# Optimization experiments

Measured on AMD Instinct MI355X. Metric: run time of the kernel, lower is better.

The kernel has to match this reference:

```python
import jax, jax.numpy as jnp
import numpy as np

DIM = 768
HEADS = 12
HEAD_DIM = DIM // HEADS


def setup_inputs() -> dict:
    key = jax.random.key(0)
    ks = jax.random.split(key, 6)
    B, N = 8, 1024
    x = jax.random.normal(ks[0], (B, N, DIM), dtype=jnp.float32)
    # Linear weights stored as (in, out) so y = x @ W + b (equiv to torch x @ W.T)
    w_qkv = jax.random.normal(ks[1], (DIM, 3 * DIM), dtype=jnp.float32) * 0.02
    b_qkv = jnp.zeros((3 * DIM,), dtype=jnp.float32)
    w_proj = jax.random.normal(ks[2], (DIM, DIM), dtype=jnp.float32) * 0.02
    b_proj = jnp.zeros((DIM,), dtype=jnp.float32)
    temperature = jnp.ones((HEADS, 1, 1), dtype=jnp.float32)
    return {"x": x, "w_qkv": w_qkv, "b_qkv": b_qkv, "w_proj": w_proj,
            "b_proj": b_proj, "temperature": temperature}


def reference(x, w_qkv, b_qkv, w_proj, b_proj, temperature):
    B, N, C = x.shape
    qkv = x @ w_qkv + b_qkv                                  # (B,N,3C)
    qkv = qkv.reshape(B, N, 3, HEADS, HEAD_DIM)
    q = qkv[:, :, 0].transpose(0, 2, 1, 3)                    # (B,H,N,D)
    k = qkv[:, :, 1].transpose(0, 2, 1, 3)
    v = qkv[:, :, 2].transpose(0, 2, 1, 3)
    # LSA: learnable per-head temperature instead of 1/sqrt(d)
    scores = jnp.einsum('bhnd,bhmd->bhnm', q, k) * temperature  # temp broadcasts over (h,1,1)
    # diagonal mask: no self-attention
    diag = jnp.eye(N, dtype=bool)
    scores = jnp.where(diag, -jnp.inf, scores)
    attn = jax.nn.softmax(scores, axis=-1)                    # dropout p=0 (eval)
    out = jnp.einsum('bhnm,bhmd->bhnd', attn, v)              # (B,H,N,D)
    out = out.transpose(0, 2, 1, 3).reshape(B, N, C)
    return out @ w_proj + b_proj
```

## Files before the change

kernel.cpp:

```cpp
#include <hip/hip_runtime.h>
#include <hip/hip_bf16.h>


typedef __attribute__((ext_vector_type(8))) short bf16x8;
typedef __attribute__((ext_vector_type(4))) float f32x4;

__device__ __forceinline__ unsigned short f2bf(float f) {
    union { float f; unsigned u; } v; v.f = f;
    unsigned r = v.u + 0x7fff + ((v.u >> 16) & 1);
    return (unsigned short)(r >> 16);
}

__device__ __forceinline__ void gl_lds16(const unsigned short* g, unsigned short* l) {
    __builtin_amdgcn_global_load_lds(
        (const __attribute__((address_space(1))) void*)g,
        (__attribute__((address_space(3))) void*)l, 16, 0, 0);
}

__device__ __forceinline__ bf16x8 rd_sw(const unsigned short* lds, int row, int chunk) {
    return *(const bf16x8*)&lds[row * 64 + (((chunk ^ (row & 7))) << 3)];
}

__device__ __forceinline__ void stage64(const unsigned short* g, int gstride,
                                        unsigned short* lds, int t) {
    int row0 = t >> 3, c = t & 7;
    #pragma unroll
    for (int r = 0; r < 2; r++) {
        int row = r * 32 + row0;
        gl_lds16(g + (size_t)row * gstride + ((c ^ (row & 7)) << 3),
                 lds + r * 2048 + ((t >> 6) << 9));
    }
}

__global__ void pack_x(const float* __restrict__ src, unsigned short* __restrict__ dst, int n4) {
    int i = blockIdx.x * blockDim.x + threadIdx.x;
    if (i < n4) {
        float4 v = ((const float4*)src)[i];
        ushort4 o;
        o.x = f2bf(v.x); o.y = f2bf(v.y); o.z = f2bf(v.z); o.w = f2bf(v.w);
        ((ushort4*)dst)[i] = o;
    }
}

__global__ void transpose_pack(const float* __restrict__ src, unsigned short* __restrict__ dst,
                               int R, int C) {
    __shared__ float tile[64][65];
    int t = threadIdx.x;
    int c0 = blockIdx.x * 64, r0 = blockIdx.y * 64;
    int tr = t >> 4, tc4 = (t & 15) * 4;
    #pragma unroll
    for (int p = 0; p < 4; p++) {
        int r = tr + p * 16;
        float4 v = *(const float4*)&src[(size_t)(r0 + r) * C + c0 + tc4];
        tile[r][tc4 + 0] = v.x; tile[r][tc4 + 1] = v.y;
        tile[r][tc4 + 2] = v.z; tile[r][tc4 + 3] = v.w;
    }
    __syncthreads();
    #pragma unroll
    for (int p = 0; p < 4; p++) {
        int rr = tr + p * 16;
        ushort4 o;
        o.x = f2bf(tile[tc4 + 0][rr]);
        o.y = f2bf(tile[tc4 + 1][rr]);
        o.z = f2bf(tile[tc4 + 2][rr]);
        o.w = f2bf(tile[tc4 + 3][rr]);
        *(ushort4*)&dst[(size_t)(c0 + rr) * R + r0 + tc4] = o;
    }
}

__global__ __launch_bounds__(256, 2)
void gemm_qkv(const unsigned short* __restrict__ xb, const unsigned short* __restrict__ wT,
              const float* __restrict__ bias,
              unsigned short* __restrict__ qb, unsigned short* __restrict__ kb,
              unsigned short* __restrict__ vb) {
    const int K = 768;
    __shared__ unsigned short As[8192];
    __shared__ unsigned short Bs[8192];
    int t = threadIdx.x;
    int m0 = blockIdx.x * 128;
    int n0 = blockIdx.y * 128;
    int w = t >> 6, lane = t & 63, l16 = lane & 15, quad = lane >> 4;
    int wm = w >> 1, wn = w & 1;
    const f32x4 zero4 = {0.f, 0.f, 0.f, 0.f};
    f32x4 acc[4][4];
    #pragma unroll
    for (int a = 0; a < 4; a++)
        #pragma unroll
        for (int b = 0; b < 4; b++) acc[a][b] = zero4;

    int row0 = t >> 3, ch = t & 7;
    const unsigned short* gA = xb + (size_t)m0 * K;
    const unsigned short* gB = wT + (size_t)n0 * K;

    for (int k0 = 0; k0 < K; k0 += 64) {
        __syncthreads();
        #pragma unroll
        for (int r = 0; r < 4; r++) {
            int row = r * 32 + row0;
            int gc = k0 + ((ch ^ (row & 7)) << 3);
            gl_lds16(gA + (size_t)row * K + gc, As + r * 2048 + ((t >> 6) << 9));
            gl_lds16(gB + (size_t)row * K + gc, Bs + r * 2048 + ((t >> 6) << 9));
        }
        __syncthreads();
        #pragma unroll
        for (int ks = 0; ks < 2; ks++) {
            bf16x8 af[4], bf[4];
            #pragma unroll
            for (int mi = 0; mi < 4; mi++)
                af[mi] = rd_sw(As, wm * 64 + mi * 16 + l16, ks * 4 + quad);
            #pragma unroll
            for (int ni = 0; ni < 4; ni++)
                bf[ni] = rd_sw(Bs, wn * 64 + ni * 16 + l16, ks * 4 + quad);
            #pragma unroll
            for (int mi = 0; mi < 4; mi++)
                #pragma unroll
                for (int ni = 0; ni < 4; ni++)
                    acc[mi][ni] = __builtin_amdgcn_mfma_f32_16x16x32_bf16(af[mi], bf[ni], acc[mi][ni], 0, 0, 0);
        }
    }

    int nb = n0 + wn * 64;
    int seg = nb / 768;
    int nc = nb % 768;
    int h = nc >> 6;
    int bb = m0 >> 10;
    int bh = bb * 12 + h;
    float bv[4];
    #pragma unroll
    for (int ni = 0; ni < 4; ni++) bv[ni] = bias[nb + ni * 16 + l16];

    if (seg < 2) {
        unsigned short* dst = (seg == 0) ? qb : kb;
        #pragma unroll
        for (int mi = 0; mi < 4; mi++) {
            int nrow_base = (m0 & 1023) + wm * 64 + mi * 16 + quad * 4;
            #pragma unroll
            for (int i = 0; i < 4; i++) {
                unsigned short* drow = dst + ((size_t)bh * 1024 + nrow_base + i) * 64;
                #pragma unroll
                for (int ni = 0; ni < 4; ni++)
                    drow[ni * 16 + l16] = f2bf(acc[mi][ni][i] + bv[ni]);
            }
        }
    } else {
        #pragma unroll
        for (int mi = 0; mi < 4; mi++) {
            int nrow0 = (m0 & 1023) + wm * 64 + mi * 16 + quad * 4;
            #pragma unroll
            for (int ni = 0; ni < 4; ni++) {
                int d = ni * 16 + l16;
                ushort4 pk;
                pk.x = f2bf(acc[mi][ni][0] + bv[ni]);
                pk.y = f2bf(acc[mi][ni][1] + bv[ni]);
                pk.z = f2bf(acc[mi][ni][2] + bv[ni]);
                pk.w = f2bf(acc[mi][ni][3] + bv[ni]);
                *(ushort4*)&vb[((size_t)bh * 64 + d) * 1024 + nrow0] = pk;
            }
        }
    }
}

__global__ __launch_bounds__(256, 4)
void attn_kernel(const unsigned short* __restrict__ qb, const unsigned short* __restrict__ kb,
                 const unsigned short* __restrict__ vb, const float* __restrict__ temp,
                 unsigned short* __restrict__ attn) {
    __shared__ unsigned short Kt[2][4096];
    __shared__ unsigned short Vt[2][4096];
    __shared__ unsigned short Ps[4][1024];
    int t = threadIdx.x, w = t >> 6, lane = t & 63, l16 = lane & 15, quad = lane >> 4;
    int bh = blockIdx.x, qblk = blockIdx.y;
    int bb = bh / 12, h = bh % 12;
    float tscale = temp[h] * 1.44269504088896f;
    int qbase = qblk * 64 + w * 16;

    const unsigned short* kbase = kb + (size_t)bh * 65536;
    const unsigned short* vbase = vb + (size_t)bh * 65536;

    stage64(kbase, 64, Kt[0], t);
    stage64(vbase, 1024, Vt[0], t);

    const unsigned short* qrow = qb + ((size_t)bh * 1024 + qbase + l16) * 64;
    bf16x8 bq0 = *(const bf16x8*)&qrow[quad * 8];
    bf16x8 bq1 = *(const bf16x8*)&qrow[32 + quad * 8];

    bf16x8 aone;
    #pragma unroll
    for (int j = 0; j < 8; j++) aone[j] = (short)0x3F80;

    const f32x4 zero4 = {0.f, 0.f, 0.f, 0.f};
    f32x4 Oacc[4];
    f32x4 Osum = zero4;
    #pragma unroll
    for (int ti = 0; ti < 4; ti++) Oacc[ti] = zero4;

    unsigned short* pw = Ps[w];

    int bw_[4];
    #pragma unroll
    for (int ni = 0; ni < 4; ni++) {
        int qp = ni * 2 + (quad >> 1);
        bw_[ni] = qp * 128 + ((l16 + 2 * qp) & 15) * 8 + (quad & 1) * 4;
    }
    int qp0 = quad, qp1 = 4 + quad;
    int br0 = qp0 * 128 + ((l16 + 2 * qp0) & 15) * 8;
    int br1 = qp1 * 128 + ((l16 + 2 * qp1) & 15) * 8;

    bool eq[4];
    #pragma unroll
    for (int i = 0; i < 4; i++) eq[i] = (l16 == quad * 4 + i);

    for (int kt = 0; kt < 16; kt++) {
        int cur = kt & 1;
        __syncthreads();
        if (kt < 15) {
            stage64(kbase + (size_t)(kt + 1) * 4096, 64, Kt[cur ^ 1], t);
            stage64(vbase + (size_t)(kt + 1) * 64, 1024, Vt[cur ^ 1], t);
        }
        const unsigned short* Kc = Kt[cur];
        const unsigned short* Vc = Vt[cur];

        #pragma unroll
        for (int ni = 0; ni < 4; ni++) {
            bf16x8 ak0 = rd_sw(Kc, ni * 16 + l16, quad);
            bf16x8 ak1 = rd_sw(Kc, ni * 16 + l16, 4 + quad);
            f32x4 z = zero4;
            z = __builtin_amdgcn_mfma_f32_16x16x32_bf16(ak0, bq0, z, 0, 0, 0);
            z = __builtin_amdgcn_mfma_f32_16x16x32_bf16(ak1, bq1, z, 0, 0, 0);
            bool dw = (kt == qblk) && (ni == w);
            float p0 = exp2f(z[0] * tscale);
            float p1 = exp2f(z[1] * tscale);
            float p2 = exp2f(z[2] * tscale);
            float p3 = exp2f(z[3] * tscale);
            if (dw) {
                if (eq[0]) p0 = 0.f;
                if (eq[1]) p1 = 0.f;
                if (eq[2]) p2 = 0.f;
                if (eq[3]) p3 = 0.f;
            }
            union { ushort4 u; __hip_bfloat162 h[2]; } pk;
            pk.h[0] = __float22bfloat162_rn(make_float2(p0, p1));
            pk.h[1] = __float22bfloat162_rn(make_float2(p2, p3));
            *(ushort4*)&pw[bw_[ni]] = pk.u;
        }

        bf16x8 pt0 = *(const bf16x8*)&pw[br0];
        bf16x8 pt1 = *(const bf16x8*)&pw[br1];

        Osum = __builtin_amdgcn_mfma_f32_16x16x32_bf16(aone, pt0, Osum, 0, 0, 0);
        Osum = __builtin_amdgcn_mfma_f32_16x16x32_bf16(aone, pt1, Osum, 0, 0, 0);

        #pragma unroll
        for (int ti = 0; ti < 4; ti++) {
            bf16x8 av0 = rd_sw(Vc, ti * 16 + l16, quad);
            bf16x8 av1 = rd_sw(Vc, ti * 16 + l16, 4 + quad);
            Oacc[ti] = __builtin_amdgcn_mfma_f32_16x16x32_bf16(av0, pt0, Oacc[ti], 0, 0, 0);
            Oacc[ti] = __builtin_amdgcn_mfma_f32_16x16x32_bf16(av1, pt1, Oacc[ti], 0, 0, 0);
        }
    }

    float inv = 1.0f / Osum[0];
    int orow = bb * 1024 + qbase + l16;
    #pragma unroll
    for (int ti = 0; ti < 4; ti++) {
        union { ushort4 u; __hip_bfloat162 h[2]; } pk;
        pk.h[0] = __float22bfloat162_rn(make_float2(Oacc[ti][0] * inv, Oacc[ti][1] * inv));
        pk.h[1] = __float22bfloat162_rn(make_float2(Oacc[ti][2] * inv, Oacc[ti][3] * inv));
        int col = h * 64 + ti * 16 + quad * 4;
        *(ushort4*)&attn[(size_t)orow * 768 + col] = pk.u;
    }
}

__global__ __launch_bounds__(256, 2)
void gemm_proj(const unsigned short* __restrict__ ab, const unsigned short* __restrict__ wT,
               const float* __restrict__ bias, float* __restrict__ out) {
    const int K = 768;
    __shared__ unsigned short As[8192];
    __shared__ unsigned short Bs[8192];
    int t = threadIdx.x;
    int m0 = blockIdx.x * 128;
    int n0 = blockIdx.y * 128;
    int w = t >> 6, lane = t & 63, l16 = lane & 15, quad = lane >> 4;
    int wm = w >> 1, wn = w & 1;
    const f32x4 zero4 = {0.f, 0.f, 0.f, 0.f};
    f32x4 acc[4][4];
    #pragma unroll
    for (int a = 0; a < 4; a++)
        #pragma unroll
        for (int b = 0; b < 4; b++) acc[a][b] = zero4;

    int row0 = t >> 3, ch = t & 7;
    const unsigned short* gA = ab + (size_t)m0 * K;
    const unsigned short* gB = wT + (size_t)n0 * K;

    for (int k0 = 0; k0 < K; k0 += 64) {
        __syncthreads();
        #pragma unroll
        for (int r = 0; r < 4; r++) {
            int row = r * 32 + row0;
            int gc = k0 + ((ch ^ (row & 7)) << 3);
            gl_lds16(gA + (size_t)row * K + gc, As + r * 2048 + ((t >> 6) << 9));
            gl_lds16(gB + (size_t)row * K + gc, Bs + r * 2048 + ((t >> 6) << 9));
        }
        __syncthreads();
        #pragma unroll
        for (int ks = 0; ks < 2; ks++) {
            bf16x8 af[4], bf[4];
            #pragma unroll
            for (int mi = 0; mi < 4; mi++)
                af[mi] = rd_sw(As, wm * 64 + mi * 16 + l16, ks * 4 + quad);
            #pragma unroll
            for (int ni = 0; ni < 4; ni++)
                bf[ni] = rd_sw(Bs, wn * 64 + ni * 16 + l16, ks * 4 + quad);
            #pragma unroll
            for (int mi = 0; mi < 4; mi++)
                #pragma unroll
                for (int ni = 0; ni < 4; ni++)
                    acc[mi][ni] = __builtin_amdgcn_mfma_f32_16x16x32_bf16(af[mi], bf[ni], acc[mi][ni], 0, 0, 0);
        }
    }

    #pragma unroll
    for (int mi = 0; mi < 4; mi++)
        #pragma unroll
        for (int i = 0; i < 4; i++) {
            int row = m0 + wm * 64 + mi * 16 + quad * 4 + i;
            float* orow = out + (size_t)row * 768;
            #pragma unroll
            for (int ni = 0; ni < 4; ni++) {
                int col = n0 + wn * 64 + ni * 16 + l16;
                orow[col] = acc[mi][ni][i] + bias[col];
            }
        }
}

extern "C" void kernel_launch(void* const* d_in, const int* in_sizes, int n_in,
                              void* d_out, int out_size, void* d_ws, size_t ws_size,
                              hipStream_t stream) {
    const float* x      = (const float*)d_in[0];
    const float* w_qkv  = (const float*)d_in[1];
    const float* b_qkv  = (const float*)d_in[2];
    const float* w_proj = (const float*)d_in[3];
    const float* b_proj = (const float*)d_in[4];
    const float* temp   = (const float*)d_in[5];
    float* out = (float*)d_out;

    char* ws = (char*)d_ws;
    unsigned short* xb     = (unsigned short*)(ws);
    unsigned short* wqkvT  = (unsigned short*)(ws + 12582912);
    unsigned short* wprojT = (unsigned short*)(ws + 16121856);
    unsigned short* qb     = (unsigned short*)(ws + 17301504);
    unsigned short* kb     = (unsigned short*)(ws + 29884416);
    unsigned short* vb     = (unsigned short*)(ws + 42467328);
    unsigned short* attn   = (unsigned short*)(ws + 55050240);

    pack_x<<<6144, 256, 0, stream>>>(x, xb, 1572864);
    transpose_pack<<<dim3(36, 12), 256, 0, stream>>>(w_qkv, wqkvT, 768, 2304);
    transpose_pack<<<dim3(12, 12), 256, 0, stream>>>(w_proj, wprojT, 768, 768);
    gemm_qkv<<<dim3(64, 18), 256, 0, stream>>>(xb, wqkvT, b_qkv, qb, kb, vb);
    attn_kernel<<<dim3(96, 16), 256, 0, stream>>>(qb, kb, vb, temp, attn);
    gemm_proj<<<dim3(64, 6), 256, 0, stream>>>(attn, wprojT, b_proj, out);
}
```

Baseline: 208.2 us.

## Keep softmax probabilities in registers, double query rows per warp, fuse prep kernels

The attention kernel now keeps the exponentiated scores in registers as the MFMA B operand instead of round-tripping them through LDS. To make that register layout line up, V columns are written permuted in the QKV GEMM. Each warp now handles 32 query rows, so every K/V tile staged in LDS is reused twice, and the grid halves. The temperature and log2e scale are folded into Q at the QKV GEMM epilogue, and the three input pack kernels are merged into one launch. The risks are higher register pressure in the attention kernel and fewer blocks in flight.

Result: faster. 188.2 us (-9.6%).

```diff
diff --git a/kernel.cpp b/kernel.cpp
--- a/kernel.cpp
+++ b/kernel.cpp
@@ -11,6 +11,12 @@
     return (unsigned short)(r >> 16);
 }
 
+__device__ __forceinline__ unsigned pack2(float a, float b) {
+    union { __hip_bfloat162 h; unsigned u; } c;
+    c.h = __float22bfloat162_rn(make_float2(a, b));
+    return c.u;
+}
+
 __device__ __forceinline__ void gl_lds16(const unsigned short* g, unsigned short* l) {
     __builtin_amdgcn_global_load_lds(
         (const __attribute__((address_space(1))) void*)g,
@@ -32,21 +38,24 @@
     }
 }
 
-__global__ void pack_x(const float* __restrict__ src, unsigned short* __restrict__ dst, int n4) {
-    int i = blockIdx.x * blockDim.x + threadIdx.x;
-    if (i < n4) {
-        float4 v = ((const float4*)src)[i];
+__global__ void prep(const float* __restrict__ x, const float* __restrict__ w_qkv,
+                     const float* __restrict__ w_proj,
+                     unsigned short* __restrict__ xb, unsigned short* __restrict__ wqkvT,
+                     unsigned short* __restrict__ wprojT) {
+    int b = blockIdx.x, t = threadIdx.x;
+    if (b < 6144) {
+        int i = b * 256 + t;
+        float4 v = ((const float4*)x)[i];
         ushort4 o;
         o.x = f2bf(v.x); o.y = f2bf(v.y); o.z = f2bf(v.z); o.w = f2bf(v.w);
-        ((ushort4*)dst)[i] = o;
-    }
-}
-
-__global__ void transpose_pack(const float* __restrict__ src, unsigned short* __restrict__ dst,
-                               int R, int C) {
+        ((ushort4*)xb)[i] = o;
+        return;
+    }
+    const float* src; unsigned short* dst; int R, C, bx, by;
+    if (b < 6576) { int b2 = b - 6144; src = w_qkv; dst = wqkvT; R = 768; C = 2304; bx = b2 % 36; by = b2 / 36; }
+    else          { int b3 = b - 6576; src = w_proj; dst = wprojT; R = 768; C = 768;  bx = b3 % 12; by = b3 / 12; }
     __shared__ float tile[64][65];
-    int t = threadIdx.x;
-    int c0 = blockIdx.x * 64, r0 = blockIdx.y * 64;
+    int c0 = bx * 64, r0 = by * 64;
     int tr = t >> 4, tc4 = (t & 15) * 4;
     #pragma unroll
     for (int p = 0; p < 4; p++) {
@@ -70,7 +79,7 @@
 
 __global__ __launch_bounds__(256, 2)
 void gemm_qkv(const unsigned short* __restrict__ xb, const unsigned short* __restrict__ wT,
-              const float* __restrict__ bias,
+              const float* __restrict__ bias, const float* __restrict__ temp,
               unsigned short* __restrict__ qb, unsigned short* __restrict__ kb,
               unsigned short* __restrict__ vb) {
     const int K = 768;
@@ -131,6 +140,7 @@
 
     if (seg < 2) {
         unsigned short* dst = (seg == 0) ? qb : kb;
+        float scale = (seg == 0) ? temp[h] * 1.44269504088896f : 1.0f;
         #pragma unroll
         for (int mi = 0; mi < 4; mi++) {
             int nrow_base = (m0 & 1023) + wm * 64 + mi * 16 + quad * 4;
@@ -139,13 +149,15 @@
                 unsigned short* drow = dst + ((size_t)bh * 1024 + nrow_base + i) * 64;
                 #pragma unroll
                 for (int ni = 0; ni < 4; ni++)
-                    drow[ni * 16 + l16] = f2bf(acc[mi][ni][i] + bv[ni]);
+                    drow[ni * 16 + l16] = f2bf((acc[mi][ni][i] + bv[ni]) * scale);
             }
         }
     } else {
         #pragma unroll
         for (int mi = 0; mi < 4; mi++) {
             int nrow0 = (m0 & 1023) + wm * 64 + mi * 16 + quad * 4;
+            int nl = nrow0 & 63;
+            int ncol = (nrow0 & 960) + (nl & 32) + ((nl & 12) << 1) + ((nl & 16) >> 2);
             #pragma unroll
             for (int ni = 0; ni < 4; ni++) {
                 int d = ni * 16 + l16;
@@ -154,7 +166,7 @@
                 pk.y = f2bf(acc[mi][ni][1] + bv[ni]);
                 pk.z = f2bf(acc[mi][ni][2] + bv[ni]);
                 pk.w = f2bf(acc[mi][ni][3] + bv[ni]);
-                *(ushort4*)&vb[((size_t)bh * 64 + d) * 1024 + nrow0] = pk;
+                *(ushort4*)&vb[((size_t)bh * 64 + d) * 1024 + ncol] = pk;
             }
         }
     }
@@ -162,16 +174,14 @@
 
 __global__ __launch_bounds__(256, 4)
 void attn_kernel(const unsigned short* __restrict__ qb, const unsigned short* __restrict__ kb,
-                 const unsigned short* __restrict__ vb, const float* __restrict__ temp,
+                 const unsigned short* __restrict__ vb,
                  unsigned short* __restrict__ attn) {
     __shared__ unsigned short Kt[2][4096];
     __shared__ unsigned short Vt[2][4096];
-    __shared__ unsigned short Ps[4][1024];
     int t = threadIdx.x, w = t >> 6, lane = t & 63, l16 = lane & 15, quad = lane >> 4;
     int bh = blockIdx.x, qblk = blockIdx.y;
     int bb = bh / 12, h = bh % 12;
-    float tscale = temp[h] * 1.44269504088896f;
-    int qbase = qblk * 64 + w * 16;
+    int qbase = qblk * 128 + w * 32;
 
     const unsigned short* kbase = kb + (size_t)bh * 65536;
     const unsigned short* vbase = vb + (size_t)bh * 65536;
@@ -179,32 +189,29 @@
     stage64(kbase, 64, Kt[0], t);
     stage64(vbase, 1024, Vt[0], t);
 
-    const unsigned short* qrow = qb + ((size_t)bh * 1024 + qbase + l16) * 64;
-    bf16x8 bq0 = *(const bf16x8*)&qrow[quad * 8];
-    bf16x8 bq1 = *(const bf16x8*)&qrow[32 + quad * 8];
+    bf16x8 bq[2][2];
+    #pragma unroll
+    for (int qh = 0; qh < 2; qh++) {
+        const unsigned short* qrow = qb + ((size_t)bh * 1024 + qbase + qh * 16 + l16) * 64;
+        bq[qh][0] = *(const bf16x8*)&qrow[quad * 8];
+        bq[qh][1] = *(const bf16x8*)&qrow[32 + quad * 8];
+    }
 
     bf16x8 aone;
     #pragma unroll
     for (int j = 0; j < 8; j++) aone[j] = (short)0x3F80;
 
     const f32x4 zero4 = {0.f, 0.f, 0.f, 0.f};
-    f32x4 Oacc[4];
-    f32x4 Osum = zero4;
-    #pragma unroll
-    for (int ti = 0; ti < 4; ti++) Oacc[ti] = zero4;
-
-    unsigned short* pw = Ps[w];
-
-    int bw_[4];
-    #pragma unroll
-    for (int ni = 0; ni < 4; ni++) {
-        int qp = ni * 2 + (quad >> 1);
-        bw_[ni] = qp * 128 + ((l16 + 2 * qp) & 15) * 8 + (quad & 1) * 4;
-    }
-    int qp0 = quad, qp1 = 4 + quad;
-    int br0 = qp0 * 128 + ((l16 + 2 * qp0) & 15) * 8;
-    int br1 = qp1 * 128 + ((l16 + 2 * qp1) & 15) * 8;
-
+    f32x4 Oacc[2][4];
+    f32x4 Osum[2];
+    #pragma unroll
+    for (int qh = 0; qh < 2; qh++) {
+        Osum[qh] = zero4;
+        #pragma unroll
+        for (int ti = 0; ti < 4; ti++) Oacc[qh][ti] = zero4;
+    }
+
+    int ktd = qbase >> 6;
     bool eq[4];
     #pragma unroll
     for (int i = 0; i < 4; i++) eq[i] = (l16 == quad * 4 + i);
@@ -219,54 +226,68 @@
         const unsigned short* Kc = Kt[cur];
         const unsigned short* Vc = Vt[cur];
 
+        unsigned pk[2][4][2];
         #pragma unroll
         for (int ni = 0; ni < 4; ni++) {
             bf16x8 ak0 = rd_sw(Kc, ni * 16 + l16, quad);
             bf16x8 ak1 = rd_sw(Kc, ni * 16 + l16, 4 + quad);
-            f32x4 z = zero4;
-            z = __builtin_amdgcn_mfma_f32_16x16x32_bf16(ak0, bq0, z, 0, 0, 0);
-            z = __builtin_amdgcn_mfma_f32_16x16x32_bf16(ak1, bq1, z, 0, 0, 0);
-            bool dw = (kt == qblk) && (ni == w);
-            float p0 = exp2f(z[0] * tscale);
-            float p1 = exp2f(z[1] * tscale);
-            float p2 = exp2f(z[2] * tscale);
-            float p3 = exp2f(z[3] * tscale);
-            if (dw) {
-                if (eq[0]) p0 = 0.f;
-                if (eq[1]) p1 = 0.f;
-                if (eq[2]) p2 = 0.f;
-                if (eq[3]) p3 = 0.f;
-            }
-            union { ushort4 u; __hip_bfloat162 h[2]; } pk;
-            pk.h[0] = __float22bfloat162_rn(make_float2(p0, p1));
-            pk.h[1] = __float22bfloat162_rn(make_float2(p2, p3));
-            *(ushort4*)&pw[bw_[ni]] = pk.u;
-        }
-
-        bf16x8 pt0 = *(const bf16x8*)&pw[br0];
-        bf16x8 pt1 = *(const bf16x8*)&pw[br1];
-
-        Osum = __builtin_amdgcn_mfma_f32_16x16x32_bf16(aone, pt0, Osum, 0, 0, 0);
-        Osum = __builtin_amdgcn_mfma_f32_16x16x32_bf16(aone, pt1, Osum, 0, 0, 0);
+            #pragma unroll
+            for (int qh = 0; qh < 2; qh++) {
+                f32x4 z = zero4;
+                z = __builtin_amdgcn_mfma_f32_16x16x32_bf16(ak0, bq[qh][0], z, 0, 0, 0);
+                z = __builtin_amdgcn_mfma_f32_16x16x32_bf16(ak1, bq[qh][1], z, 0, 0, 0);
+                float p0 = exp2f(z[0]);
+                float p1 = exp2f(z[1]);
+                float p2 = exp2f(z[2]);
+                float p3 = exp2f(z[3]);
+                if (kt == ktd && ni == ((w * 2 + qh) & 3)) {
+                    if (eq[0]) p0 = 0.f;
+                    if (eq[1]) p1 = 0.f;
+                    if (eq[2]) p2 = 0.f;
+                    if (eq[3]) p3 = 0.f;
+                }
+                pk[qh][ni][0] = pack2(p0, p1);
+                pk[qh][ni][1] = pack2(p2, p3);
+            }
+        }
+
+        union { unsigned u[4]; bf16x8 b; } pt[2][2];
+        #pragma unroll
+        for (int qh = 0; qh < 2; qh++) {
+            pt[qh][0].u[0] = pk[qh][0][0]; pt[qh][0].u[1] = pk[qh][0][1];
+            pt[qh][0].u[2] = pk[qh][1][0]; pt[qh][0].u[3] = pk[qh][1][1];
+            pt[qh][1].u[0] = pk[qh][2][0]; pt[qh][1].u[1] = pk[qh][2][1];
+            pt[qh][1].u[2] = pk[qh][3][0]; pt[qh][1].u[3] = pk[qh][3][1];
+            Osum[qh] = __builtin_amdgcn_mfma_f32_16x16x32_bf16(aone, pt[qh][0].b, Osum[qh], 0, 0, 0);
+            Osum[qh] = __builtin_amdgcn_mfma_f32_16x16x32_bf16(aone, pt[qh][1].b, Osum[qh], 0, 0, 0);
+        }
 
         #pragma unroll
         for (int ti = 0; ti < 4; ti++) {
             bf16x8 av0 = rd_sw(Vc, ti * 16 + l16, quad);
             bf16x8 av1 = rd_sw(Vc, ti * 16 + l16, 4 + quad);
-            Oacc[ti] = __builtin_amdgcn_mfma_f32_16x16x32_bf16(av0, pt0, Oacc[ti], 0, 0, 0);
-            Oacc[ti] = __builtin_amdgcn_mfma_f32_16x16x32_bf16(av1, pt1, Oacc[ti], 0, 0, 0);
-        }
-    }
-
-    float inv = 1.0f / Osum[0];
-    int orow = bb * 1024 + qbase + l16;
-    #pragma unroll
-    for (int ti = 0; ti < 4; ti++) {
-        union { ushort4 u; __hip_bfloat162 h[2]; } pk;
-        pk.h[0] = __float22bfloat162_rn(make_float2(Oacc[ti][0] * inv, Oacc[ti][1] * inv));
-        pk.h[1] = __float22bfloat162_rn(make_float2(Oacc[ti][2] * inv, Oacc[ti][3] * inv));
-        int col = h * 64 + ti * 16 + quad * 4;
-        *(ushort4*)&attn[(size_t)orow * 768 + col] = pk.u;
+            #pragma unroll
+            for (int qh = 0; qh < 2; qh++) {
+                Oacc[qh][ti] = __builtin_amdgcn_mfma_f32_16x16x32_bf16(av0, pt[qh][0].b, Oacc[qh][ti], 0, 0, 0);
+                Oacc[qh][ti] = __builtin_amdgcn_mfma_f32_16x16x32_bf16(av1, pt[qh][1].b, Oacc[qh][ti], 0, 0, 0);
+            }
+        }
+    }
+
+    #pragma unroll
+    for (int qh = 0; qh < 2; qh++) {
+        float inv = 1.0f / Osum[qh][0];
+        int orow = bb * 1024 + qbase + qh * 16 + l16;
+        #pragma unroll
+        for (int ti = 0; ti < 4; ti++) {
+            ushort4 pk4;
+            pk4.x = (unsigned short)(pack2(Oacc[qh][ti][0] * inv, Oacc[qh][ti][1] * inv) & 0xffff);
+            pk4.y = (unsigned short)(pack2(Oacc[qh][ti][0] * inv, Oacc[qh][ti][1] * inv) >> 16);
+            pk4.z = (unsigned short)(pack2(Oacc[qh][ti][2] * inv, Oacc[qh][ti][3] * inv) & 0xffff);
+            pk4.w = (unsigned short)(pack2(Oacc[qh][ti][2] * inv, Oacc[qh][ti][3] * inv) >> 16);
+            int col = h * 64 + ti * 16 + quad * 4;
+            *(ushort4*)&attn[(size_t)orow * 768 + col] = pk4;
+        }
     }
 }
 
@@ -353,10 +374,8 @@
     unsigned short* vb     = (unsigned short*)(ws + 42467328);
     unsigned short* attn   = (unsigned short*)(ws + 55050240);
 
-    pack_x<<<6144, 256, 0, stream>>>(x, xb, 1572864);
-    transpose_pack<<<dim3(36, 12), 256, 0, stream>>>(w_qkv, wqkvT, 768, 2304);
-    transpose_pack<<<dim3(12, 12), 256, 0, stream>>>(w_proj, wprojT, 768, 768);
-    gemm_qkv<<<dim3(64, 18), 256, 0, stream>>>(xb, wqkvT, b_qkv, qb, kb, vb);
-    attn_kernel<<<dim3(96, 16), 256, 0, stream>>>(qb, kb, vb, temp, attn);
+    prep<<<6720, 256, 0, stream>>>(x, w_qkv, w_proj, xb, wqkvT, wprojT);
+    gemm_qkv<<<dim3(64, 18), 256, 0, stream>>>(xb, wqkvT, b_qkv, temp, qb, kb, vb);
+    attn_kernel<<<dim3(96, 8), 256, 0, stream>>>(qb, kb, vb, attn);
     gemm_proj<<<dim3(64, 6), 256, 0, stream>>>(attn, wprojT, b_proj, out);
 }
```
